# Kernel tuning notes

Hardware: AMD Instinct MI355X
Metric: run time of the kernel (lower is better)

## Reference

```python
import jax, jax.numpy as jnp
import numpy as np
import math

E = 8        # num_experts
L2 = 15
L3 = 32
D = 3072     # eval_features_per_perspective
R = 256      # router_features
B = 16384
AUX_ALPHA = 0.01
Z_ALPHA = 0.001


def setup_inputs() -> dict:
    key = jax.random.key(0)
    ks = jax.random.split(key, 12)
    inp = {
        "expert_input": jax.random.uniform(ks[0], (B, D), jnp.float32),
        "router_input": jax.random.normal(ks[1], (R,) , jnp.float32) * 0 + jax.random.normal(ks[1], (B, R), jnp.float32),
        # router init: normal(std=0.01), zero bias (as in _reset_router)
        "router_w": jax.random.normal(ks[2], (E, R), jnp.float32) * 0.01,
        "router_b": jnp.zeros((E,), jnp.float32),
        # FactorizedStackedLinear l1: stacked weight [E*(L2+1), D] + shared factorized [(L2+1), D]
        "l1_w": jax.random.normal(ks[3], (E * (L2 + 1), D), jnp.float32) * (1.0 / math.sqrt(D)),
        "l1_b": jax.random.normal(ks[4], (E * (L2 + 1),), jnp.float32) * 0.01,
        "l1f_w": jax.random.normal(ks[5], (L2 + 1, D), jnp.float32) * (1.0 / math.sqrt(D)),
        "l1f_b": jax.random.normal(ks[6], (L2 + 1,), jnp.float32) * 0.01,
        # StackedLinear l2: [E*L3, 2*L2]
        "l2_w": jax.random.normal(ks[7], (E * L3, 2 * L2), jnp.float32) * (1.0 / math.sqrt(2 * L2)),
        "l2_b": jax.random.normal(ks[8], (E * L3,), jnp.float32) * 0.01,
        # StackedLinear output: [E*1, L3], bias zeroed in __init__
        "out_w": jax.random.normal(ks[9], (E, L3), jnp.float32) * (1.0 / math.sqrt(L3)),
        "out_b": jnp.zeros((E,), jnp.float32),
    }
    return inp


def reference(expert_input, router_input, router_w, router_b,
              l1_w, l1_b, l1f_w, l1f_b, l2_w, l2_b, out_w, out_b):
    # ---- router + straight-through hard gate ----
    gate_logits = router_input @ router_w.T + router_b                      # [B, E]
    gate_probs = jax.nn.softmax(gate_logits, axis=-1)
    expert_indices = jnp.argmax(gate_logits, axis=-1)                       # [B]
    hard_gate = jax.nn.one_hot(expert_indices, E, dtype=gate_probs.dtype)   # [B, E]
    gate = hard_gate + gate_probs - jax.lax.stop_gradient(gate_probs)

    # ---- routing metrics / losses ----
    fraction_routed = hard_gate.mean(axis=0)                                 # [E]
    avg_gate_prob = gate_probs.mean(axis=0)                                  # [E]
    aux_loss = E * jnp.sum(fraction_routed * avg_gate_prob)
    z_loss = jnp.mean(jnp.square(jax.nn.logsumexp(gate_logits, axis=-1)))
    entropy = jnp.mean(-jnp.sum(gate_probs * jnp.log(jnp.clip(gate_probs, 1e-9)), axis=-1))
    normalized_entropy = entropy / jnp.float32(math.log(max(E, 2)))
    top1_prob = jnp.mean(jnp.max(gate_probs, axis=-1))
    router_loss = jnp.float32(AUX_ALPHA) * aux_loss + jnp.float32(Z_ALPHA) * z_loss  # training path

    # ---- l1: FactorizedStackedLinear, dense over all experts (training path) ----
    merged_w = (l1_w + jnp.tile(l1f_w, (E, 1))).reshape(E, L2 + 1, D)        # [E, L2+1, D]
    merged_b = (l1_b + jnp.tile(l1f_b, (E,))).reshape(E, L2 + 1)             # [E, L2+1]
    l1c = jnp.einsum('bi,eoi->beo', expert_input, merged_w) + merged_b[None]  # [B, E, L2+1]
    l1x, l1x_out = l1c[:, :, :L2], l1c[:, :, L2:]                            # [B,E,L2], [B,E,1]
    l1x = jnp.clip(jnp.concatenate([jnp.square(l1x) * (255.0 / 256.0), l1x], axis=2), 0.0, 1.0)  # [B,E,2*L2]

    # ---- l2 + output StackedLinear ----
    w2 = l2_w.reshape(E, L3, 2 * L2)
    l2x = jnp.clip(jnp.einsum('bei,eoi->beo', l1x, w2) + l2_b.reshape(E, L3)[None], 0.0, 1.0)  # [B,E,L3]
    wo = out_w.reshape(E, 1, L3)
    l3x = jnp.einsum('bei,eoi->beo', l2x, wo) + out_b.reshape(E, 1)[None] + l1x_out            # [B,E,1]

    # ---- gated combine ----
    out = jnp.einsum('be,beo->bo', gate, l3x)                                # [B, 1]
    return (out, router_loss, aux_loss, z_loss, fraction_routed, avg_gate_prob,
            normalized_entropy, top1_prob)
```

## Files before the change

kernel.cpp:

```cpp
#include <hip/hip_runtime.h>

constexpr int NB  = 16384;
constexpr int ND  = 3072;
constexpr int NR  = 256;
constexpr int NE  = 8;
constexpr int NO1 = 16;
constexpr int NL2D = 30;
constexpr int NL3 = 32;

constexpr size_t WS_CURSORS = 32;
constexpr size_t WS_OFFPAD  = 128;
constexpr size_t WS_IDX     = 256;
constexpr size_t WS_BUCKET  = WS_IDX + (size_t)NB*4;
constexpr size_t WS_MB      = WS_BUCKET + (size_t)(NB+256)*4;
constexpr size_t WS_MW      = WS_MB + 512;
constexpr size_t WS_BLK_CNT  = WS_MW + (size_t)128*3072*4;
constexpr size_t WS_BLK_SUMP = WS_BLK_CNT + 8192;
constexpr size_t WS_BLK_Z    = WS_BLK_SUMP + 8192;
constexpr size_t WS_BLK_ENT  = WS_BLK_Z + 1024;
constexpr size_t WS_BLK_TOP  = WS_BLK_ENT + 1024;

__device__ __forceinline__ float clamp01(float v) { return fminf(fmaxf(v, 0.0f), 1.0f); }

__device__ __forceinline__ void stage16(const float* g, float* l) {
    __builtin_amdgcn_global_load_lds(
        (const __attribute__((address_space(1))) unsigned int*)g,
        (__attribute__((address_space(3))) unsigned int*)l,
        16, 0, 0);
}

__global__ __launch_bounds__(256) void router2_kernel(
    const float* __restrict__ rin, const float* __restrict__ rw,
    const float* __restrict__ rb, int* __restrict__ idx,
    int* __restrict__ blk_cnt, float* __restrict__ blk_sump,
    float* __restrict__ blk_z, float* __restrict__ blk_ent, float* __restrict__ blk_top)
{
    __shared__ float w_s[NE][NR];
    __shared__ float red_f[4][11];
    __shared__ int   red_c[4][8];

    const int t = threadIdx.x;
    {
        const float4* src = (const float4*)rw;
        float4* dst = (float4*)&w_s[0][0];
        dst[t]       = src[t];
        dst[t + 256] = src[t + 256];
    }
    __syncthreads();

    const int q  = t & 3;
    const int rr = t >> 2;
    const int b  = blockIdx.x * 64 + rr;
    const float* rp = rin + (size_t)b * NR + q * 64;

    float acc[NE];
#pragma unroll
    for (int e = 0; e < NE; ++e) acc[e] = 0.0f;

#pragma unroll
    for (int c = 0; c < 16; ++c) {
        const float4 xv = *(const float4*)(rp + c * 4);
#pragma unroll
        for (int e = 0; e < NE; ++e) {
            const float4 wv = *(const float4*)(&w_s[e][q * 64 + c * 4]);
            acc[e] = fmaf(xv.x, wv.x, acc[e]);
            acc[e] = fmaf(xv.y, wv.y, acc[e]);
            acc[e] = fmaf(xv.z, wv.z, acc[e]);
            acc[e] = fmaf(xv.w, wv.w, acc[e]);
        }
    }
    float lg[NE];
#pragma unroll
    for (int e = 0; e < NE; ++e) {
        float v = acc[e];
        v += __shfl_xor(v, 1);
        v += __shfl_xor(v, 2);
        lg[e] = v + rb[e];
    }

    float m = lg[0]; int am = 0;
#pragma unroll
    for (int e = 1; e < NE; ++e) { if (lg[e] > m) { m = lg[e]; am = e; } }
    float p[NE]; float ssum = 0.0f;
#pragma unroll
    for (int e = 0; e < NE; ++e) { p[e] = __expf(lg[e] - m); ssum += p[e]; }
    const float inv = 1.0f / ssum;
    const float lse = m + __logf(ssum);

    const bool active = (q == 0);
    float sv[11];
    float ent = 0.0f, top = 0.0f;
#pragma unroll
    for (int e = 0; e < NE; ++e) {
        const float pj = p[e] * inv;
        sv[e] = pj;
        ent -= pj * __logf(fmaxf(pj, 1e-9f));
        top = fmaxf(top, pj);
    }
    sv[8] = lse * lse;
    sv[9] = ent;
    sv[10] = top;
    if (!active) {
#pragma unroll
        for (int i = 0; i < 11; ++i) sv[i] = 0.0f;
    }
    if (active) idx[b] = am;

#pragma unroll
    for (int i = 0; i < 11; ++i) {
        float v = sv[i];
        v += __shfl_xor(v, 4);
        v += __shfl_xor(v, 8);
        v += __shfl_xor(v, 16);
        v += __shfl_xor(v, 32);
        sv[i] = v;
    }
    int cnt[NE];
#pragma unroll
    for (int j = 0; j < NE; ++j) {
        unsigned long long mk = __ballot(active && (am == j));
        cnt[j] = __popcll(mk);
    }

    const int wave = t >> 6;
    if ((t & 63) == 0) {
#pragma unroll
        for (int i = 0; i < 11; ++i) red_f[wave][i] = sv[i];
#pragma unroll
        for (int j = 0; j < NE; ++j) red_c[wave][j] = cnt[j];
    }
    __syncthreads();

    const int bid = blockIdx.x;
    if (t < 8) {
        blk_sump[bid * 8 + t] = red_f[0][t] + red_f[1][t] + red_f[2][t] + red_f[3][t];
        blk_cnt [bid * 8 + t] = red_c[0][t] + red_c[1][t] + red_c[2][t] + red_c[3][t];
    } else if (t == 8) {
        blk_z[bid]   = red_f[0][8] + red_f[1][8] + red_f[2][8] + red_f[3][8];
    } else if (t == 9) {
        blk_ent[bid] = red_f[0][9] + red_f[1][9] + red_f[2][9] + red_f[3][9];
    } else if (t == 10) {
        blk_top[bid] = red_f[0][10] + red_f[1][10] + red_f[2][10] + red_f[3][10];
    }
}

__global__ __launch_bounds__(256) void merge_kernel(
    const float* __restrict__ l1w, const float* __restrict__ l1b,
    const float* __restrict__ l1fw, const float* __restrict__ l1fb,
    float* __restrict__ mw, float* __restrict__ mb)
{
    const int i = blockIdx.x * 256 + threadIdx.x;
    const int total = NE * NO1 * ND;
    if (i < total) {
        mw[i] = l1w[i] + l1fw[i % (NO1 * ND)];
    }
    if (i < NE * NO1) {
        mb[i] = l1b[i] + l1fb[i & (NO1 - 1)];
    }
}

__global__ __launch_bounds__(256) void finalize2_kernel(
    const int* __restrict__ blk_cnt, const float* __restrict__ blk_sump,
    const float* __restrict__ blk_z, const float* __restrict__ blk_ent,
    const float* __restrict__ blk_top, int* __restrict__ offpad,
    float* __restrict__ out)
{
    __shared__ float ps_s[32][8];
    __shared__ int   pc_s[32][8];
    __shared__ float zet_s[3][4];
    __shared__ float tot_f[8];
    __shared__ int   tot_c[8];

    const int t = threadIdx.x;
    {
        const int e = t & 7, g = t >> 3;
        float ps = 0.0f; int pc = 0;
#pragma unroll
        for (int k = 0; k < 8; ++k) {
            const int bb = g * 8 + k;
            ps += blk_sump[bb * 8 + e];
            pc += blk_cnt [bb * 8 + e];
        }
        ps_s[g][e] = ps;
        pc_s[g][e] = pc;
    }
    {
        float z = blk_z[t], en = blk_ent[t], tp = blk_top[t];
#pragma unroll
        for (int o = 1; o < 64; o <<= 1) {
            z  += __shfl_xor(z, o);
            en += __shfl_xor(en, o);
            tp += __shfl_xor(tp, o);
        }
        const int wave = t >> 6;
        if ((t & 63) == 0) { zet_s[0][wave] = z; zet_s[1][wave] = en; zet_s[2][wave] = tp; }
    }
    __syncthreads();

    if (t < 8) {
        float s = 0.0f; int c = 0;
        for (int g = 0; g < 32; ++g) { s += ps_s[g][t]; c += pc_s[g][t]; }
        tot_f[t] = s; tot_c[t] = c;
    }
    __syncthreads();

    if (t == 0) {
        int run = 0;
#pragma unroll
        for (int e = 0; e < NE; ++e) {
            offpad[e] = run;
            run += (tot_c[e] + 31) & ~31;
        }
        offpad[NE] = run;

        const float invB = 1.0f / (float)NB;
        float aux = 0.0f;
        float frac[NE], avg[NE];
#pragma unroll
        for (int e = 0; e < NE; ++e) {
            frac[e] = (float)tot_c[e] * invB;
            avg[e]  = tot_f[e] * invB;
            aux += frac[e] * avg[e];
        }
        aux *= (float)NE;
        const float z   = (zet_s[0][0] + zet_s[0][1] + zet_s[0][2] + zet_s[0][3]) * invB;
        const float ent = (zet_s[1][0] + zet_s[1][1] + zet_s[1][2] + zet_s[1][3]) * invB;
        const float top = (zet_s[2][0] + zet_s[2][1] + zet_s[2][2] + zet_s[2][3]) * invB;
        const float rl  = 0.01f * aux + 0.001f * z;

        float* o = out + NB;
        o[0] = rl;
        o[1] = aux;
        o[2] = z;
#pragma unroll
        for (int e = 0; e < NE; ++e) o[3 + e]  = frac[e];
#pragma unroll
        for (int e = 0; e < NE; ++e) o[11 + e] = avg[e];
        o[19] = ent / __logf(8.0f);
        o[20] = top;
    }
}

__global__ __launch_bounds__(256) void scatter_kernel(
    const int* __restrict__ idx, const int* __restrict__ offpad,
    int* __restrict__ cursors, int* __restrict__ bucket)
{
    const int b = blockIdx.x * 256 + threadIdx.x;
    const int e = idx[b];
    const int lane = threadIdx.x & 63;
#pragma unroll
    for (int ee = 0; ee < NE; ++ee) {
        unsigned long long mask = __ballot(e == ee);
        if (e == ee) {
            int leader = __ffsll((unsigned long long)mask) - 1;
            int cnt = __popcll(mask);
            int base = 0;
            if (lane == leader) base = atomicAdd(&cursors[ee], cnt);
            base = __shfl(base, leader);
            int pos = base + __popcll(mask & ((1ull << lane) - 1ull));
            bucket[offpad[ee] + pos] = b;
        }
    }
}

__global__ __launch_bounds__(256) void moe_main_kernel(
    const float* __restrict__ x, const float* __restrict__ mw,
    const float* __restrict__ mb, const float* __restrict__ l2w,
    const float* __restrict__ l2b, const float* __restrict__ ow,
    const float* __restrict__ ob, const int* __restrict__ bucket,
    const int* __restrict__ offpad, float* __restrict__ out)
{
    __shared__ float x_lds[2][8][128];
    __shared__ int   rows_s[8];
    __shared__ int   expert_s;
    __shared__ float l1c_s[8][16];
    __shared__ float l1x_s[8][30];
    __shared__ float l1c15_s[8];

    const int t = threadIdx.x;
    const int slot0 = blockIdx.x * 8;
    if (t < 8) rows_s[t] = bucket[slot0 + t];
    if (t == 0) {
        int e = 0;
#pragma unroll
        for (int j = 1; j < NE; ++j) if (slot0 >= offpad[j]) e = j;
        expert_s = e;
    }
    __syncthreads();

    const int e    = expert_s;
    const int wid  = t >> 6;
    const int lane = t & 63;
    const int half = lane >> 5;
    const int s    = lane & 31;
    const int rgrp = half;

    int srow = rows_s[2 * wid + half];
    if (srow < 0) srow = 0;
    const float* stage_src = x + (size_t)srow * ND + s * 4;
    float* stage_dst0 = &x_lds[0][2 * wid][0];
    float* stage_dst1 = &x_lds[1][2 * wid][0];

    const float* wbase = mw + (size_t)e * NO1 * ND + (size_t)(4 * wid) * ND;

    float acc[4][4];
#pragma unroll
    for (int rr = 0; rr < 4; ++rr)
#pragma unroll
        for (int oo = 0; oo < 4; ++oo) acc[rr][oo] = 0.0f;

    stage16(stage_src, stage_dst0);
    __syncthreads();

    for (int c = 0; c < 24; ++c) {
        const int cur = c & 1;
        if (c + 1 < 24)
            stage16(stage_src + (c + 1) * 128, cur ? stage_dst0 : stage_dst1);

        const float* wk = wbase + c * 128 + s * 4;
        const float4 wv0 = *(const float4*)(wk);
        const float4 wv1 = *(const float4*)(wk + ND);
        const float4 wv2 = *(const float4*)(wk + 2 * ND);
        const float4 wv3 = *(const float4*)(wk + 3 * ND);

        float4 xv[4];
#pragma unroll
        for (int rr = 0; rr < 4; ++rr)
            xv[rr] = *(const float4*)&x_lds[cur][rgrp * 4 + rr][s * 4];

#pragma unroll
        for (int rr = 0; rr < 4; ++rr) {
            acc[rr][0] = fmaf(xv[rr].x, wv0.x, acc[rr][0]);
            acc[rr][0] = fmaf(xv[rr].y, wv0.y, acc[rr][0]);
            acc[rr][0] = fmaf(xv[rr].z, wv0.z, acc[rr][0]);
            acc[rr][0] = fmaf(xv[rr].w, wv0.w, acc[rr][0]);
            acc[rr][1] = fmaf(xv[rr].x, wv1.x, acc[rr][1]);
            acc[rr][1] = fmaf(xv[rr].y, wv1.y, acc[rr][1]);
            acc[rr][1] = fmaf(xv[rr].z, wv1.z, acc[rr][1]);
            acc[rr][1] = fmaf(xv[rr].w, wv1.w, acc[rr][1]);
            acc[rr][2] = fmaf(xv[rr].x, wv2.x, acc[rr][2]);
            acc[rr][2] = fmaf(xv[rr].y, wv2.y, acc[rr][2]);
            acc[rr][2] = fmaf(xv[rr].z, wv2.z, acc[rr][2]);
            acc[rr][2] = fmaf(xv[rr].w, wv2.w, acc[rr][2]);
            acc[rr][3] = fmaf(xv[rr].x, wv3.x, acc[rr][3]);
            acc[rr][3] = fmaf(xv[rr].y, wv3.y, acc[rr][3]);
            acc[rr][3] = fmaf(xv[rr].z, wv3.z, acc[rr][3]);
            acc[rr][3] = fmaf(xv[rr].w, wv3.w, acc[rr][3]);
        }
        __syncthreads();
    }

#pragma unroll
    for (int rr = 0; rr < 4; ++rr)
#pragma unroll
        for (int oo = 0; oo < 4; ++oo) {
            float a = acc[rr][oo];
            a += __shfl_xor(a, 1);
            a += __shfl_xor(a, 2);
            a += __shfl_xor(a, 4);
            a += __shfl_xor(a, 8);
            a += __shfl_xor(a, 16);
            acc[rr][oo] = a;
        }
    if (s == 0) {
#pragma unroll
        for (int rr = 0; rr < 4; ++rr)
#pragma unroll
            for (int oo = 0; oo < 4; ++oo)
                l1c_s[rgrp * 4 + rr][4 * wid + oo] = acc[rr][oo];
    }
    __syncthreads();

    const int r = t >> 5;
    const int q = t & 31;
    const int rowb = rows_s[r];

    if (q < 16) {
        const int o = q;
        float v = l1c_s[r][o] + mb[e * NO1 + o];
        if (o < 15) {
            l1x_s[r][o]      = clamp01(v * v * (255.0f / 256.0f));
            l1x_s[r][o + 15] = clamp01(v);
        } else {
            l1c15_s[r] = v;
        }
    }
    __syncthreads();

    float a2 = l2b[e * NL3 + q];
    const float* w2r = l2w + (size_t)e * NL3 * NL2D + q * NL2D;
#pragma unroll
    for (int i = 0; i < NL2D; ++i) a2 = fmaf(l1x_s[r][i], w2r[i], a2);
    a2 = clamp01(a2);
    float pacc = a2 * ow[e * NL3 + q];
    pacc += __shfl_xor(pacc, 1);
    pacc += __shfl_xor(pacc, 2);
    pacc += __shfl_xor(pacc, 4);
    pacc += __shfl_xor(pacc, 8);
    pacc += __shfl_xor(pacc, 16);

    if (q == 0 && rowb >= 0) {
        out[rowb] = pacc + ob[e] + l1c15_s[r];
    }
}

extern "C" void kernel_launch(void* const* d_in, const int* in_sizes, int n_in,
                              void* d_out, int out_size, void* d_ws, size_t ws_size,
                              hipStream_t stream)
{
    const float* x    = (const float*)d_in[0];
    const float* rin  = (const float*)d_in[1];
    const float* rw   = (const float*)d_in[2];
    const float* rb   = (const float*)d_in[3];
    const float* l1w  = (const float*)d_in[4];
    const float* l1b  = (const float*)d_in[5];
    const float* l1fw = (const float*)d_in[6];
    const float* l1fb = (const float*)d_in[7];
    const float* l2w  = (const float*)d_in[8];
    const float* l2b  = (const float*)d_in[9];
    const float* ow   = (const float*)d_in[10];
    const float* ob   = (const float*)d_in[11];
    float* out = (float*)d_out;

    char* ws = (char*)d_ws;
    int*   cursors = (int*)(ws + WS_CURSORS);
    int*   offpad  = (int*)(ws + WS_OFFPAD);
    int*   idx     = (int*)(ws + WS_IDX);
    int*   bucket  = (int*)(ws + WS_BUCKET);
    float* mb      = (float*)(ws + WS_MB);
    float* mw      = (float*)(ws + WS_MW);
    int*   blk_cnt  = (int*)(ws + WS_BLK_CNT);
    float* blk_sump = (float*)(ws + WS_BLK_SUMP);
    float* blk_z    = (float*)(ws + WS_BLK_Z);
    float* blk_ent  = (float*)(ws + WS_BLK_ENT);
    float* blk_top  = (float*)(ws + WS_BLK_TOP);

    hipMemsetAsync(ws, 0, 256, stream);
    hipMemsetAsync(ws + WS_BUCKET, 0xFF, (size_t)(NB + 256) * 4, stream);

    router2_kernel<<<NB / 64, 256, 0, stream>>>(rin, rw, rb, idx, blk_cnt, blk_sump,
                                                blk_z, blk_ent, blk_top);
    merge_kernel<<<(NE * NO1 * ND + 255) / 256, 256, 0, stream>>>(l1w, l1b, l1fw, l1fb, mw, mb);
    finalize2_kernel<<<1, 256, 0, stream>>>(blk_cnt, blk_sump, blk_z, blk_ent, blk_top,
                                            offpad, out);
    scatter_kernel<<<NB / 256, 256, 0, stream>>>(idx, offpad, cursors, bucket);
    moe_main_kernel<<<(NB + 256) / 8, 256, 0, stream>>>(x, mw, mb, l2w, l2b, ow, ob,
                                                        bucket, offpad, out);
}
```

Baseline: 98.16 us.

## Fuse router with weight merge, scatter with finalize, and stage weights via LDS

The router and l1 weight-merge kernels become one launch, with extra blocks doing a float4 merge. Finalize and scatter become one launch: each scatter block recomputes the expert offsets from the per-block counts, while one extra block writes the loss metrics. Together this cuts five launches to three and removes serial dependencies. The main kernel now double-buffers its l1 weight tiles into LDS with async global-to-LDS loads instead of direct global float4 reads, at the cost of more shared memory per block.

```diff
diff --git a/kernel.cpp b/kernel.cpp
--- a/kernel.cpp
+++ b/kernel.cpp
@@ -29,17 +29,34 @@
         16, 0, 0);
 }
 
-__global__ __launch_bounds__(256) void router2_kernel(
+__global__ __launch_bounds__(256) void router_merge_kernel(
     const float* __restrict__ rin, const float* __restrict__ rw,
     const float* __restrict__ rb, int* __restrict__ idx,
     int* __restrict__ blk_cnt, float* __restrict__ blk_sump,
-    float* __restrict__ blk_z, float* __restrict__ blk_ent, float* __restrict__ blk_top)
+    float* __restrict__ blk_z, float* __restrict__ blk_ent, float* __restrict__ blk_top,
+    const float* __restrict__ l1w, const float* __restrict__ l1b,
+    const float* __restrict__ l1fw, const float* __restrict__ l1fb,
+    float* __restrict__ mw, float* __restrict__ mb)
 {
+    const int t = threadIdx.x;
+
+    if (blockIdx.x >= 256) {
+        const int gid = blockIdx.x - 256;
+        const int i4 = gid * 256 + t;
+        const float4 a = ((const float4*)l1w)[i4];
+        const float4 b = ((const float4*)l1fw)[i4 % (NO1 * ND / 4)];
+        float4 r; r.x = a.x + b.x; r.y = a.y + b.y; r.z = a.z + b.z; r.w = a.w + b.w;
+        ((float4*)mw)[i4] = r;
+        if (gid == 0 && t < NE * NO1) {
+            mb[t] = l1b[t] + l1fb[t & (NO1 - 1)];
+        }
+        return;
+    }
+
     __shared__ float w_s[NE][NR];
     __shared__ float red_f[4][11];
     __shared__ int   red_c[4][8];
 
-    const int t = threadIdx.x;
     {
         const float4* src = (const float4*)rw;
         float4* dst = (float4*)&w_s[0][0];
@@ -144,110 +161,120 @@
     }
 }
 
-__global__ __launch_bounds__(256) void merge_kernel(
-    const float* __restrict__ l1w, const float* __restrict__ l1b,
-    const float* __restrict__ l1fw, const float* __restrict__ l1fb,
-    float* __restrict__ mw, float* __restrict__ mb)
-{
-    const int i = blockIdx.x * 256 + threadIdx.x;
-    const int total = NE * NO1 * ND;
-    if (i < total) {
-        mw[i] = l1w[i] + l1fw[i % (NO1 * ND)];
-    }
-    if (i < NE * NO1) {
-        mb[i] = l1b[i] + l1fb[i & (NO1 - 1)];
-    }
-}
-
-__global__ __launch_bounds__(256) void finalize2_kernel(
+__global__ __launch_bounds__(256) void scatter_finalize_kernel(
     const int* __restrict__ blk_cnt, const float* __restrict__ blk_sump,
     const float* __restrict__ blk_z, const float* __restrict__ blk_ent,
-    const float* __restrict__ blk_top, int* __restrict__ offpad,
-    float* __restrict__ out)
+    const float* __restrict__ blk_top, const int* __restrict__ idx,
+    int* __restrict__ cursors, int* __restrict__ bucket,
+    int* __restrict__ offpad, float* __restrict__ out)
 {
-    __shared__ float ps_s[32][8];
-    __shared__ int   pc_s[32][8];
-    __shared__ float zet_s[3][4];
-    __shared__ float tot_f[8];
-    __shared__ int   tot_c[8];
-
     const int t = threadIdx.x;
+
+    if (blockIdx.x == 64) {
+        __shared__ float ps_s[32][8];
+        __shared__ int   pc_s[32][8];
+        __shared__ float zet_s[3][4];
+        __shared__ float tot_f[8];
+        __shared__ int   tot_c[8];
+        {
+            const int e = t & 7, g = t >> 3;
+            float ps = 0.0f; int pc = 0;
+#pragma unroll
+            for (int k = 0; k < 8; ++k) {
+                const int bb = g * 8 + k;
+                ps += blk_sump[bb * 8 + e];
+                pc += blk_cnt [bb * 8 + e];
+            }
+            ps_s[g][e] = ps;
+            pc_s[g][e] = pc;
+        }
+        {
+            float z = blk_z[t], en = blk_ent[t], tp = blk_top[t];
+#pragma unroll
+            for (int o = 1; o < 64; o <<= 1) {
+                z  += __shfl_xor(z, o);
+                en += __shfl_xor(en, o);
+                tp += __shfl_xor(tp, o);
+            }
+            const int wave = t >> 6;
+            if ((t & 63) == 0) { zet_s[0][wave] = z; zet_s[1][wave] = en; zet_s[2][wave] = tp; }
+        }
+        __syncthreads();
+        if (t < 8) {
+            float s = 0.0f; int c = 0;
+            for (int g = 0; g < 32; ++g) { s += ps_s[g][t]; c += pc_s[g][t]; }
+            tot_f[t] = s; tot_c[t] = c;
+        }
+        __syncthreads();
+        if (t == 0) {
+            int run = 0;
+#pragma unroll
+            for (int e = 0; e < NE; ++e) {
+                offpad[e] = run;
+                run += (tot_c[e] + 31) & ~31;
+            }
+            offpad[NE] = run;
+
+            const float invB = 1.0f / (float)NB;
+            float aux = 0.0f;
+            float frac[NE], avg[NE];
+#pragma unroll
+            for (int e = 0; e < NE; ++e) {
+                frac[e] = (float)tot_c[e] * invB;
+                avg[e]  = tot_f[e] * invB;
+                aux += frac[e] * avg[e];
+            }
+            aux *= (float)NE;
+            const float z   = (zet_s[0][0] + zet_s[0][1] + zet_s[0][2] + zet_s[0][3]) * invB;
+            const float ent = (zet_s[1][0] + zet_s[1][1] + zet_s[1][2] + zet_s[1][3]) * invB;
+            const float top = (zet_s[2][0] + zet_s[2][1] + zet_s[2][2] + zet_s[2][3]) * invB;
+            const float rl  = 0.01f * aux + 0.001f * z;
+
+            float* o = out + NB;
+            o[0] = rl;
+            o[1] = aux;
+            o[2] = z;
+#pragma unroll
+            for (int e = 0; e < NE; ++e) o[3 + e]  = frac[e];
+#pragma unroll
+            for (int e = 0; e < NE; ++e) o[11 + e] = avg[e];
+            o[19] = ent / __logf(8.0f);
+            o[20] = top;
+        }
+        return;
+    }
+
+    __shared__ int red_c[4][8];
+    __shared__ int offp[8];
     {
-        const int e = t & 7, g = t >> 3;
-        float ps = 0.0f; int pc = 0;
-#pragma unroll
-        for (int k = 0; k < 8; ++k) {
-            const int bb = g * 8 + k;
-            ps += blk_sump[bb * 8 + e];
-            pc += blk_cnt [bb * 8 + e];
-        }
-        ps_s[g][e] = ps;
-        pc_s[g][e] = pc;
-    }
-    {
-        float z = blk_z[t], en = blk_ent[t], tp = blk_top[t];
-#pragma unroll
-        for (int o = 1; o < 64; o <<= 1) {
-            z  += __shfl_xor(z, o);
-            en += __shfl_xor(en, o);
-            tp += __shfl_xor(tp, o);
+        const int4 a = ((const int4*)blk_cnt)[t * 2];
+        const int4 bql = ((const int4*)blk_cnt)[t * 2 + 1];
+        int v[8] = {a.x, a.y, a.z, a.w, bql.x, bql.y, bql.z, bql.w};
+#pragma unroll
+        for (int j = 0; j < 8; ++j) {
+#pragma unroll
+            for (int o = 1; o < 64; o <<= 1) v[j] += __shfl_xor(v[j], o);
         }
         const int wave = t >> 6;
-        if ((t & 63) == 0) { zet_s[0][wave] = z; zet_s[1][wave] = en; zet_s[2][wave] = tp; }
-    }
-    __syncthreads();
-
-    if (t < 8) {
-        float s = 0.0f; int c = 0;
-        for (int g = 0; g < 32; ++g) { s += ps_s[g][t]; c += pc_s[g][t]; }
-        tot_f[t] = s; tot_c[t] = c;
-    }
-    __syncthreads();
-
+        if ((t & 63) == 0) {
+#pragma unroll
+            for (int j = 0; j < 8; ++j) red_c[wave][j] = v[j];
+        }
+    }
+    __syncthreads();
     if (t == 0) {
         int run = 0;
 #pragma unroll
         for (int e = 0; e < NE; ++e) {
-            offpad[e] = run;
-            run += (tot_c[e] + 31) & ~31;
-        }
-        offpad[NE] = run;
-
-        const float invB = 1.0f / (float)NB;
-        float aux = 0.0f;
-        float frac[NE], avg[NE];
-#pragma unroll
-        for (int e = 0; e < NE; ++e) {
-            frac[e] = (float)tot_c[e] * invB;
-            avg[e]  = tot_f[e] * invB;
-            aux += frac[e] * avg[e];
-        }
-        aux *= (float)NE;
-        const float z   = (zet_s[0][0] + zet_s[0][1] + zet_s[0][2] + zet_s[0][3]) * invB;
-        const float ent = (zet_s[1][0] + zet_s[1][1] + zet_s[1][2] + zet_s[1][3]) * invB;
-        const float top = (zet_s[2][0] + zet_s[2][1] + zet_s[2][2] + zet_s[2][3]) * invB;
-        const float rl  = 0.01f * aux + 0.001f * z;
-
-        float* o = out + NB;
-        o[0] = rl;
-        o[1] = aux;
-        o[2] = z;
-#pragma unroll
-        for (int e = 0; e < NE; ++e) o[3 + e]  = frac[e];
-#pragma unroll
-        for (int e = 0; e < NE; ++e) o[11 + e] = avg[e];
-        o[19] = ent / __logf(8.0f);
-        o[20] = top;
-    }
-}
-
-__global__ __launch_bounds__(256) void scatter_kernel(
-    const int* __restrict__ idx, const int* __restrict__ offpad,
-    int* __restrict__ cursors, int* __restrict__ bucket)
-{
-    const int b = blockIdx.x * 256 + threadIdx.x;
+            offp[e] = run;
+            run += (red_c[0][e] + red_c[1][e] + red_c[2][e] + red_c[3][e] + 31) & ~31;
+        }
+    }
+    __syncthreads();
+
+    const int b = blockIdx.x * 256 + t;
     const int e = idx[b];
-    const int lane = threadIdx.x & 63;
+    const int lane = t & 63;
 #pragma unroll
     for (int ee = 0; ee < NE; ++ee) {
         unsigned long long mask = __ballot(e == ee);
@@ -258,7 +285,7 @@
             if (lane == leader) base = atomicAdd(&cursors[ee], cnt);
             base = __shfl(base, leader);
             int pos = base + __popcll(mask & ((1ull << lane) - 1ull));
-            bucket[offpad[ee] + pos] = b;
+            bucket[offp[ee] + pos] = b;
         }
     }
 }
@@ -271,6 +298,7 @@
     const int* __restrict__ offpad, float* __restrict__ out)
 {
     __shared__ float x_lds[2][8][128];
+    __shared__ float w_lds[2][16][128];
     __shared__ int   rows_s[8];
     __shared__ int   expert_s;
     __shared__ float l1c_s[8][16];
@@ -293,15 +321,13 @@
     const int lane = t & 63;
     const int half = lane >> 5;
     const int s    = lane & 31;
-    const int rgrp = half;
 
     int srow = rows_s[2 * wid + half];
     if (srow < 0) srow = 0;
-    const float* stage_src = x + (size_t)srow * ND + s * 4;
-    float* stage_dst0 = &x_lds[0][2 * wid][0];
-    float* stage_dst1 = &x_lds[1][2 * wid][0];
-
-    const float* wbase = mw + (size_t)e * NO1 * ND + (size_t)(4 * wid) * ND;
+    const float* xsrc = x + (size_t)srow * ND + s * 4;
+    const float* wbase = mw + (size_t)e * NO1 * ND;
+    const float* wsrc0 = wbase + (size_t)(4 * wid + 0 + half) * ND + s * 4;
+    const float* wsrc1 = wbase + (size_t)(4 * wid + 2 + half) * ND + s * 4;
 
     float acc[4][4];
 #pragma unroll
@@ -309,43 +335,40 @@
 #pragma unroll
         for (int oo = 0; oo < 4; ++oo) acc[rr][oo] = 0.0f;
 
-    stage16(stage_src, stage_dst0);
+    stage16(xsrc,  &x_lds[0][2 * wid][0]);
+    stage16(wsrc0, &w_lds[0][4 * wid][0]);
+    stage16(wsrc1, &w_lds[0][4 * wid + 2][0]);
     __syncthreads();
 
     for (int c = 0; c < 24; ++c) {
         const int cur = c & 1;
-        if (c + 1 < 24)
-            stage16(stage_src + (c + 1) * 128, cur ? stage_dst0 : stage_dst1);
-
-        const float* wk = wbase + c * 128 + s * 4;
-        const float4 wv0 = *(const float4*)(wk);
-        const float4 wv1 = *(const float4*)(wk + ND);
-        const float4 wv2 = *(const float4*)(wk + 2 * ND);
-        const float4 wv3 = *(const float4*)(wk + 3 * ND);
-
-        float4 xv[4];
+        const int nxt = cur ^ 1;
+        if (c + 1 < 24) {
+            const int off = (c + 1) * 128;
+            stage16(xsrc + off,  &x_lds[nxt][2 * wid][0]);
+            stage16(wsrc0 + off, &w_lds[nxt][4 * wid][0]);
+            stage16(wsrc1 + off, &w_lds[nxt][4 * wid + 2][0]);
+        }
+
+        float4 xv[4], wv[4];
 #pragma unroll
         for (int rr = 0; rr < 4; ++rr)
-            xv[rr] = *(const float4*)&x_lds[cur][rgrp * 4 + rr][s * 4];
+            xv[rr] = *(const float4*)&x_lds[cur][half * 4 + rr][s * 4];
+#pragma unroll
+        for (int oo = 0; oo < 4; ++oo)
+            wv[oo] = *(const float4*)&w_lds[cur][4 * wid + oo][s * 4];
 
 #pragma unroll
         for (int rr = 0; rr < 4; ++rr) {
-            acc[rr][0] = fmaf(xv[rr].x, wv0.x, acc[rr][0]);
-            acc[rr][0] = fmaf(xv[rr].y, wv0.y, acc[rr][0]);
-            acc[rr][0] = fmaf(xv[rr].z, wv0.z, acc[rr][0]);
-            acc[rr][0] = fmaf(xv[rr].w, wv0.w, acc[rr][0]);
-            acc[rr][1] = fmaf(xv[rr].x, wv1.x, acc[rr][1]);
-            acc[rr][1] = fmaf(xv[rr].y, wv1.y, acc[rr][1]);
-            acc[rr][1] = fmaf(xv[rr].z, wv1.z, acc[rr][1]);
-            acc[rr][1] = fmaf(xv[rr].w, wv1.w, acc[rr][1]);
-            acc[rr][2] = fmaf(xv[rr].x, wv2.x, acc[rr][2]);
-            acc[rr][2] = fmaf(xv[rr].y, wv2.y, acc[rr][2]);
-            acc[rr][2] = fmaf(xv[rr].z, wv2.z, acc[rr][2]);
-            acc[rr][2] = fmaf(xv[rr].w, wv2.w, acc[rr][2]);
-            acc[rr][3] = fmaf(xv[rr].x, wv3.x, acc[rr][3]);
-            acc[rr][3] = fmaf(xv[rr].y, wv3.y, acc[rr][3]);
-            acc[rr][3] = fmaf(xv[rr].z, wv3.z, acc[rr][3]);
-            acc[rr][3] = fmaf(xv[rr].w, wv3.w, acc[rr][3]);
+#pragma unroll
+            for (int oo = 0; oo < 4; ++oo) {
+                float a = acc[rr][oo];
+                a = fmaf(xv[rr].x, wv[oo].x, a);
+                a = fmaf(xv[rr].y, wv[oo].y, a);
+                a = fmaf(xv[rr].z, wv[oo].z, a);
+                a = fmaf(xv[rr].w, wv[oo].w, a);
+                acc[rr][oo] = a;
+            }
         }
         __syncthreads();
     }
@@ -367,7 +390,7 @@
         for (int rr = 0; rr < 4; ++rr)
 #pragma unroll
             for (int oo = 0; oo < 4; ++oo)
-                l1c_s[rgrp * 4 + rr][4 * wid + oo] = acc[rr][oo];
+                l1c_s[half * 4 + rr][4 * wid + oo] = acc[rr][oo];
     }
     __syncthreads();
 
@@ -438,12 +461,12 @@
     hipMemsetAsync(ws, 0, 256, stream);
     hipMemsetAsync(ws + WS_BUCKET, 0xFF, (size_t)(NB + 256) * 4, stream);
 
-    router2_kernel<<<NB / 64, 256, 0, stream>>>(rin, rw, rb, idx, blk_cnt, blk_sump,
-                                                blk_z, blk_ent, blk_top);
-    merge_kernel<<<(NE * NO1 * ND + 255) / 256, 256, 0, stream>>>(l1w, l1b, l1fw, l1fb, mw, mb);
-    finalize2_kernel<<<1, 256, 0, stream>>>(blk_cnt, blk_sump, blk_z, blk_ent, blk_top,
-                                            offpad, out);
-    scatter_kernel<<<NB / 256, 256, 0, stream>>>(idx, offpad, cursors, bucket);
+    router_merge_kernel<<<640, 256, 0, stream>>>(rin, rw, rb, idx, blk_cnt, blk_sump,
+                                                 blk_z, blk_ent, blk_top,
+                                                 l1w, l1b, l1fw, l1fb, mw, mb);
+    scatter_finalize_kernel<<<65, 256, 0, stream>>>(blk_cnt, blk_sump, blk_z, blk_ent,
+                                                    blk_top, idx, cursors, bucket,
+                                                    offpad, out);
     moe_main_kernel<<<(NB + 256) / 8, 256, 0, stream>>>(x, mw, mb, l2w, l2b, ow, ob,
                                                         bucket, offpad, out);
 }
```

Measured after the change: 99.07 us. About the same (+0.9%).
